# Optimization experiments

Hardware: AMD Instinct MI355X
Metric: run time of the kernel (lower is better)

The kernel has to match this reference:

```python
import jax, jax.numpy as jnp
import numpy as np

K = 3  # kernel size


def _bilinear_sample(x, px, py):
    """Bilinear sample x:[b,c,h,w] at pixel coords px,py:[b,t,h,w].
    Zeros padding, align_corners=True semantics (coords are raw pixel coords).
    Returns [b,c,t,h,w]."""
    b, c, h, w = x.shape
    x0 = jnp.floor(px)
    y0 = jnp.floor(py)
    wx1 = px - x0
    wx0 = 1.0 - wx1
    wy1 = py - y0
    wy0 = 1.0 - wy1
    xf = x.reshape(b, c, h * w)

    def gather(xi, yi):
        valid = (xi >= 0) & (xi <= w - 1) & (yi >= 0) & (yi <= h - 1)
        xi_c = jnp.clip(xi, 0, w - 1).astype(jnp.int32)
        yi_c = jnp.clip(yi, 0, h - 1).astype(jnp.int32)
        idx = (yi_c * w + xi_c).reshape(b, 1, -1)  # [b,1,t*h*w]
        v = jnp.take_along_axis(xf, idx, axis=2).reshape(b, c, *xi.shape[1:])
        return v * valid[:, None].astype(x.dtype)

    out = (gather(x0, y0) * (wx0 * wy0)[:, None]
           + gather(x0 + 1, y0) * (wx1 * wy0)[:, None]
           + gather(x0, y0 + 1) * (wx0 * wy1)[:, None]
           + gather(x0 + 1, y0 + 1) * (wx1 * wy1)[:, None])
    return out


def setup_inputs() -> dict:
    key = jax.random.key(0)
    k1, k2, k3 = jax.random.split(key, 3)
    b, c, h, w = 4, 64, 128, 128
    out_c = 64
    x = jax.random.normal(k1, (b, c, h, w), dtype=jnp.float32)
    offset = jax.random.normal(k2, (b, 2 * K * K, h, w), dtype=jnp.float32)
    weight = jax.random.normal(k3, (out_c, c, K, K), dtype=jnp.float32) * 0.05
    bias = jnp.zeros((out_c,), dtype=jnp.float32)
    return {"x": x, "offset": offset, "weight": weight, "bias": bias}


def reference(x, offset, weight, bias):
    b, c, h, w = x.shape
    kk = K * K
    # base integer grid (x along width, y along height)
    yy, xx = jnp.meshgrid(jnp.arange(h, dtype=x.dtype), jnp.arange(w, dtype=x.dtype), indexing='ij')
    off = offset.reshape(b, kk, 2, h, w)
    # grid_sample with align_corners=True inverts the module's normalization,
    # so effective sampling coords are simply base + offset in pixel space.
    px = xx[None, None] + off[:, :, 0]  # [b,kk,h,w]
    py = yy[None, None] + off[:, :, 1]
    sampled = _bilinear_sample(x, px, py)  # [b,c,kk,h,w]
    w2 = weight.reshape(weight.shape[0], c, kk)  # [o,c,kk]
    out = jnp.einsum('oct,bcthw->bohw', w2, sampled)
    return out + bias[None, :, None, None]
```

## Files before the change

kernel.cpp:

```cpp
#include <hip/hip_runtime.h>
#include <cstddef>

#define BH 4
#define CH 64
#define OH 64
#define HH 128
#define WW 128
#define KK 9
#define HW (HH * WW)

typedef __attribute__((ext_vector_type(8))) short short8;
typedef __attribute__((ext_vector_type(4))) float f32x4;
typedef __attribute__((ext_vector_type(2))) float f32x2;
typedef __attribute__((ext_vector_type(4))) unsigned int uint4v;
typedef __attribute__((ext_vector_type(4))) unsigned short ushort4v;

__device__ __forceinline__ unsigned short f2bf(float f) {
    unsigned u = __float_as_uint(f);
    u += 0x7fffu + ((u >> 16) & 1u);
    return (unsigned short)(u >> 16);
}
__device__ __forceinline__ f32x2 bf2x2(unsigned d) {
    f32x2 r;
    r.x = __uint_as_float(d << 16);
    r.y = __uint_as_float(d & 0xffff0000u);
    return r;
}
__device__ __forceinline__ unsigned pack_bf2(f32x2 v) {
    unsigned u0 = __float_as_uint(v.x);
    u0 += 0x7fffu + ((u0 >> 16) & 1u);
    unsigned u1 = __float_as_uint(v.y);
    u1 += 0x7fffu + ((u1 >> 16) & 1u);
    return __builtin_amdgcn_perm(u1, u0, 0x07060302);
}
__device__ __forceinline__ uint4v combine4(uint4v c00, uint4v c10, uint4v c01, uint4v c11,
                                           float w00, float w10, float w01, float w11) {
    f32x2 W00 = {w00, w00}, W10 = {w10, w10}, W01 = {w01, w01}, W11 = {w11, w11};
    uint4v r;
#pragma unroll
    for (int j = 0; j < 4; ++j) {
        f32x2 s = W00 * bf2x2(c00[j]) + W10 * bf2x2(c10[j])
                + W01 * bf2x2(c01[j]) + W11 * bf2x2(c11[j]);
        r[j] = pack_bf2(s);
    }
    return r;
}

__global__ __launch_bounds__(256) void dcl_prep(const float* __restrict__ x,
                                                const float* __restrict__ wgt,
                                                unsigned short* __restrict__ xt,
                                                unsigned short* __restrict__ wtb) {
    if (blockIdx.x < 1024) {
        __shared__ float tile[64][65];
        int chunk = blockIdx.x;
        int b = chunk >> 8;
        int hw0 = (chunk & 255) * 64;
        int tid = threadIdx.x;
        int tx = tid & 63;
        int ty = tid >> 6;
        const float* xb = x + (size_t)b * CH * HW;
#pragma unroll
        for (int c = ty; c < 64; c += 4)
            tile[c][tx] = xb[(size_t)c * HW + hw0 + tx];
        __syncthreads();
        unsigned short* xtb = xt + ((size_t)b << 20);
        int c4 = (tid & 15) * 4;
        int p0 = tid >> 4;
#pragma unroll
        for (int it = 0; it < 4; ++it) {
            int pxl = p0 + it * 16;
            ushort4v v = { f2bf(tile[c4 + 0][pxl]), f2bf(tile[c4 + 1][pxl]),
                           f2bf(tile[c4 + 2][pxl]), f2bf(tile[c4 + 3][pxl]) };
            *(ushort4v*)(xtb + (size_t)(hw0 + pxl) * CH + c4) = v;
        }
    } else {
        int idx = (blockIdx.x - 1024) * 256 + threadIdx.x;
        int j  = idx & 7;
        int l  = (idx >> 3) & 63;
        int nt = (idx >> 9) & 3;
        int ks = idx >> 11;
        int k = ks * 32 + ((l >> 4) * 8) + j;
        int n = nt * 16 + (l & 15);
        int c = k & 63;
        int t = k >> 6;
        wtb[idx] = f2bf(wgt[(n * CH + c) * KK + t]);
    }
}

#define SMEM_INTS 4352

__global__ __launch_bounds__(256, 4) void dcl_main(
        const unsigned short* __restrict__ xt,
        const float* __restrict__ offset,
        const unsigned short* __restrict__ wtb,
        const float* __restrict__ bias,
        float* __restrict__ out) {
    __shared__ __align__(16) int smem[SMEM_INTS];
    int tid = threadIdx.x;
    int lane = tid & 63;
    int wave = tid >> 6;

    int b  = blockIdx.x >> 8;
    int t8 = blockIdx.x & 255;
    int x0 = (t8 & 7) << 4;
    int y0 = (t8 >> 3) << 2;
    int m = lane & 15;
    int quad = lane >> 4;
    int qoff = quad * 16;
    int y = y0 + wave;
    int pm = x0 + m;

    const char* xtb = (const char*)xt;
    const float* ob = offset + (((size_t)(b * 18)) << 14) + (y << 7) + pm;
    float pxf = (float)pm;
    float pyf = (float)y;

    float oxv[9], oyv[9];
#pragma unroll
    for (int t = 0; t < 9; ++t) {
        oxv[t] = ob[(size_t)(2 * t) << 14];
        oyv[t] = ob[(size_t)(2 * t + 1) << 14];
    }

    const uint4v* bsrc = (const uint4v*)wtb;

    {
        uint4v* dst = (uint4v*)smem;
        dst[tid]       = bsrc[tid];
        dst[tid + 256] = bsrc[tid + 256];
    }

    f32x4 acc[4];
#pragma unroll
    for (int i = 0; i < 4; ++i) acc[i] = (f32x4)(0.f);

    __syncthreads();

#pragma unroll 1
    for (int t = 0; t < 9; ++t) {
        uint4v r0, r1;
        if (t < 8) {
            r0 = bsrc[(t + 1) * 512 + tid];
            r1 = bsrc[(t + 1) * 512 + 256 + tid];
        }

        float fx = pxf + oxv[t];
        float fy = pyf + oyv[t];
        float x0f = floorf(fx), y0f = floorf(fy);
        float wx1 = fx - x0f, wy1 = fy - y0f;
        float wx0 = 1.0f - wx1, wy0 = 1.0f - wy1;
        int ix0 = (int)x0f, iy0 = (int)y0f;
        int ix1 = ix0 + 1, iy1 = iy0 + 1;
        bool vx0 = (unsigned)ix0 < (unsigned)WW;
        bool vx1 = (unsigned)ix1 < (unsigned)WW;
        bool vy0 = (unsigned)iy0 < (unsigned)HH;
        bool vy1 = (unsigned)iy1 < (unsigned)HH;
        float w00 = (vx0 && vy0) ? wx0 * wy0 : 0.0f;
        float w10 = (vx1 && vy0) ? wx1 * wy0 : 0.0f;
        float w01 = (vx0 && vy1) ? wx0 * wy1 : 0.0f;
        float w11 = (vx1 && vy1) ? wx1 * wy1 : 0.0f;
        int cx0 = min(max(ix0, 0), WW - 1), cx1 = min(max(ix1, 0), WW - 1);
        int cy0 = min(max(iy0, 0), HH - 1), cy1 = min(max(iy1, 0), HH - 1);
        int base = b << 14;
        int o00 = ((base + (cy0 << 7) + cx0) << 7) + qoff;
        int o10 = ((base + (cy0 << 7) + cx1) << 7) + qoff;
        int o01 = ((base + (cy1 << 7) + cx0) << 7) + qoff;
        int o11 = ((base + (cy1 << 7) + cx1) << 7) + qoff;

        uint4v c00a = *(const uint4v*)(xtb + o00);
        uint4v c10a = *(const uint4v*)(xtb + o10);
        uint4v c01a = *(const uint4v*)(xtb + o01);
        uint4v c11a = *(const uint4v*)(xtb + o11);
        uint4v c00b = *(const uint4v*)(xtb + o00 + 64);
        uint4v c10b = *(const uint4v*)(xtb + o10 + 64);
        uint4v c01b = *(const uint4v*)(xtb + o01 + 64);
        uint4v c11b = *(const uint4v*)(xtb + o11 + 64);
        uint4v ra = combine4(c00a, c10a, c01a, c11a, w00, w10, w01, w11);
        uint4v rb = combine4(c00b, c10b, c01b, c11b, w00, w10, w01, w11);
        short8 aa = __builtin_bit_cast(short8, ra);
        short8 ab = __builtin_bit_cast(short8, rb);

        const short8* bl = (const short8*)(smem + (t & 1) * 2048);
#pragma unroll
        for (int nt = 0; nt < 4; ++nt)
            acc[nt] = __builtin_amdgcn_mfma_f32_16x16x32_bf16(
                aa, bl[nt * 64 + lane], acc[nt], 0, 0, 0);
#pragma unroll
        for (int nt = 0; nt < 4; ++nt)
            acc[nt] = __builtin_amdgcn_mfma_f32_16x16x32_bf16(
                ab, bl[(4 + nt) * 64 + lane], acc[nt], 0, 0, 0);

        if (t < 8) {
            uint4v* dst = (uint4v*)(smem + ((t + 1) & 1) * 2048);
            dst[tid]       = r0;
            dst[tid + 256] = r1;
        }
        __syncthreads();
    }

    float* o_w = (float*)smem + wave * 1040;
#pragma unroll
    for (int nt = 0; nt < 4; ++nt)
#pragma unroll
        for (int reg = 0; reg < 4; ++reg)
            o_w[(quad * 4 + reg) * 65 + nt * 16 + m] = acc[nt][reg];
    __syncthreads();

    const float* os = (const float*)smem;
#pragma unroll
    for (int j = tid; j < 64 * 64; j += 256) {
        int o = j >> 6;
        int p = j & 63;
        int row = p >> 4, xx = p & 15;
        float v = os[row * 1040 + xx * 65 + o] + bias[o];
        out[(((size_t)(b * OH + o)) << 14) + ((y0 + row) << 7) + x0 + xx] = v;
    }
}

extern "C" void kernel_launch(void* const* d_in, const int* in_sizes, int n_in,
                              void* d_out, int out_size, void* d_ws, size_t ws_size,
                              hipStream_t stream) {
    const float* x      = (const float*)d_in[0];
    const float* offset = (const float*)d_in[1];
    const float* weight = (const float*)d_in[2];
    const float* bias   = (const float*)d_in[3];
    float* out = (float*)d_out;

    unsigned short* xt  = (unsigned short*)d_ws;
    unsigned short* wtb = (unsigned short*)((char*)d_ws + (size_t)BH * HW * CH * 2);

    dcl_prep<<<1024 + 144, 256, 0, stream>>>(x, weight, xt, wtb);
    dcl_main<<<(BH * HW) / 64, 256, 0, stream>>>(xt, offset, wtb, bias, out);
}
```

Measured before the change: 115.8 us.

## Split kernel taps across two wave groups with smem reduction of partial sums

Doubles the block to 512 threads. Two groups of four waves each handle a disjoint subset of the 9 kernel taps for the same 64 pixels: taps 0-4 and taps 5-8. Their partial accumulators are summed in shared memory during the epilogue. Offsets are now loaded one tap ahead instead of all up front, which cuts register pressure. The aim is more latency hiding for the gather loads through higher wave parallelism. The cost is a larger shared memory footprint, a load imbalance (group 1 idles on the last iteration), and an extra reduction.

Result: slower. 148.1 us (+27.9%).

```diff
diff --git a/kernel.cpp b/kernel.cpp
--- a/kernel.cpp
+++ b/kernel.cpp
@@ -87,9 +87,9 @@
     }
 }
 
-#define SMEM_INTS 4352
-
-__global__ __launch_bounds__(256, 4) void dcl_main(
+#define SMEM_INTS 8320
+
+__global__ __launch_bounds__(512, 8) void dcl_main(
         const unsigned short* __restrict__ xt,
         const float* __restrict__ offset,
         const unsigned short* __restrict__ wtb,
@@ -99,6 +99,8 @@
     int tid = threadIdx.x;
     int lane = tid & 63;
     int wave = tid >> 6;
+    int group = wave >> 2;
+    int r = wave & 3;
 
     int b  = blockIdx.x >> 8;
     int t8 = blockIdx.x & 255;
@@ -107,28 +109,25 @@
     int m = lane & 15;
     int quad = lane >> 4;
     int qoff = quad * 16;
-    int y = y0 + wave;
+    int y = y0 + r;
     int pm = x0 + m;
 
     const char* xtb = (const char*)xt;
     const float* ob = offset + (((size_t)(b * 18)) << 14) + (y << 7) + pm;
     float pxf = (float)pm;
     float pyf = (float)y;
-
-    float oxv[9], oyv[9];
-#pragma unroll
-    for (int t = 0; t < 9; ++t) {
-        oxv[t] = ob[(size_t)(2 * t) << 14];
-        oyv[t] = ob[(size_t)(2 * t + 1) << 14];
-    }
+    int t0 = group ? 5 : 0;
 
     const uint4v* bsrc = (const uint4v*)wtb;
 
     {
-        uint4v* dst = (uint4v*)smem;
-        dst[tid]       = bsrc[tid];
-        dst[tid + 256] = bsrc[tid + 256];
-    }
+        uint4v* d0 = (uint4v*)(smem);
+        uint4v* d1 = (uint4v*)(smem + 2 * 2048);
+        d0[tid] = bsrc[0 * 512 + tid];
+        d1[tid] = bsrc[5 * 512 + tid];
+    }
+    float ox_c = ob[(size_t)(2 * t0) << 14];
+    float oy_c = ob[(size_t)(2 * t0 + 1) << 14];
 
     f32x4 acc[4];
 #pragma unroll
@@ -137,64 +136,74 @@
     __syncthreads();
 
 #pragma unroll 1
-    for (int t = 0; t < 9; ++t) {
+    for (int i = 0; i < 5; ++i) {
         uint4v r0, r1;
-        if (t < 8) {
-            r0 = bsrc[(t + 1) * 512 + tid];
-            r1 = bsrc[(t + 1) * 512 + 256 + tid];
-        }
-
-        float fx = pxf + oxv[t];
-        float fy = pyf + oyv[t];
-        float x0f = floorf(fx), y0f = floorf(fy);
-        float wx1 = fx - x0f, wy1 = fy - y0f;
-        float wx0 = 1.0f - wx1, wy0 = 1.0f - wy1;
-        int ix0 = (int)x0f, iy0 = (int)y0f;
-        int ix1 = ix0 + 1, iy1 = iy0 + 1;
-        bool vx0 = (unsigned)ix0 < (unsigned)WW;
-        bool vx1 = (unsigned)ix1 < (unsigned)WW;
-        bool vy0 = (unsigned)iy0 < (unsigned)HH;
-        bool vy1 = (unsigned)iy1 < (unsigned)HH;
-        float w00 = (vx0 && vy0) ? wx0 * wy0 : 0.0f;
-        float w10 = (vx1 && vy0) ? wx1 * wy0 : 0.0f;
-        float w01 = (vx0 && vy1) ? wx0 * wy1 : 0.0f;
-        float w11 = (vx1 && vy1) ? wx1 * wy1 : 0.0f;
-        int cx0 = min(max(ix0, 0), WW - 1), cx1 = min(max(ix1, 0), WW - 1);
-        int cy0 = min(max(iy0, 0), HH - 1), cy1 = min(max(iy1, 0), HH - 1);
-        int base = b << 14;
-        int o00 = ((base + (cy0 << 7) + cx0) << 7) + qoff;
-        int o10 = ((base + (cy0 << 7) + cx1) << 7) + qoff;
-        int o01 = ((base + (cy1 << 7) + cx0) << 7) + qoff;
-        int o11 = ((base + (cy1 << 7) + cx1) << 7) + qoff;
-
-        uint4v c00a = *(const uint4v*)(xtb + o00);
-        uint4v c10a = *(const uint4v*)(xtb + o10);
-        uint4v c01a = *(const uint4v*)(xtb + o01);
-        uint4v c11a = *(const uint4v*)(xtb + o11);
-        uint4v c00b = *(const uint4v*)(xtb + o00 + 64);
-        uint4v c10b = *(const uint4v*)(xtb + o10 + 64);
-        uint4v c01b = *(const uint4v*)(xtb + o01 + 64);
-        uint4v c11b = *(const uint4v*)(xtb + o11 + 64);
-        uint4v ra = combine4(c00a, c10a, c01a, c11a, w00, w10, w01, w11);
-        uint4v rb = combine4(c00b, c10b, c01b, c11b, w00, w10, w01, w11);
-        short8 aa = __builtin_bit_cast(short8, ra);
-        short8 ab = __builtin_bit_cast(short8, rb);
-
-        const short8* bl = (const short8*)(smem + (t & 1) * 2048);
-#pragma unroll
-        for (int nt = 0; nt < 4; ++nt)
-            acc[nt] = __builtin_amdgcn_mfma_f32_16x16x32_bf16(
-                aa, bl[nt * 64 + lane], acc[nt], 0, 0, 0);
-#pragma unroll
-        for (int nt = 0; nt < 4; ++nt)
-            acc[nt] = __builtin_amdgcn_mfma_f32_16x16x32_bf16(
-                ab, bl[(4 + nt) * 64 + lane], acc[nt], 0, 0, 0);
-
-        if (t < 8) {
-            uint4v* dst = (uint4v*)(smem + ((t + 1) & 1) * 2048);
-            dst[tid]       = r0;
-            dst[tid + 256] = r1;
-        }
+        float ox_n = 0.f, oy_n = 0.f;
+        if (i < 4) {
+            r0 = bsrc[(i + 1) * 512 + tid];
+            int tg1 = (6 + i < 9) ? (6 + i) : 8;
+            r1 = bsrc[tg1 * 512 + tid];
+            int tn = t0 + i + 1;
+            if (tn > 8) tn = 8;
+            ox_n = ob[(size_t)(2 * tn) << 14];
+            oy_n = ob[(size_t)(2 * tn + 1) << 14];
+        }
+
+        if (group == 0 || i < 4) {
+            float fx = pxf + ox_c;
+            float fy = pyf + oy_c;
+            float x0f = floorf(fx), y0f = floorf(fy);
+            float wx1 = fx - x0f, wy1 = fy - y0f;
+            float wx0 = 1.0f - wx1, wy0 = 1.0f - wy1;
+            int ix0 = (int)x0f, iy0 = (int)y0f;
+            int ix1 = ix0 + 1, iy1 = iy0 + 1;
+            bool vx0 = (unsigned)ix0 < (unsigned)WW;
+            bool vx1 = (unsigned)ix1 < (unsigned)WW;
+            bool vy0 = (unsigned)iy0 < (unsigned)HH;
+            bool vy1 = (unsigned)iy1 < (unsigned)HH;
+            float w00 = (vx0 && vy0) ? wx0 * wy0 : 0.0f;
+            float w10 = (vx1 && vy0) ? wx1 * wy0 : 0.0f;
+            float w01 = (vx0 && vy1) ? wx0 * wy1 : 0.0f;
+            float w11 = (vx1 && vy1) ? wx1 * wy1 : 0.0f;
+            int cx0 = min(max(ix0, 0), WW - 1), cx1 = min(max(ix1, 0), WW - 1);
+            int cy0 = min(max(iy0, 0), HH - 1), cy1 = min(max(iy1, 0), HH - 1);
+            int base = b << 14;
+            int o00 = ((base + (cy0 << 7) + cx0) << 7) + qoff;
+            int o10 = ((base + (cy0 << 7) + cx1) << 7) + qoff;
+            int o01 = ((base + (cy1 << 7) + cx0) << 7) + qoff;
+            int o11 = ((base + (cy1 << 7) + cx1) << 7) + qoff;
+
+            uint4v c00a = *(const uint4v*)(xtb + o00);
+            uint4v c10a = *(const uint4v*)(xtb + o10);
+            uint4v c01a = *(const uint4v*)(xtb + o01);
+            uint4v c11a = *(const uint4v*)(xtb + o11);
+            uint4v c00b = *(const uint4v*)(xtb + o00 + 64);
+            uint4v c10b = *(const uint4v*)(xtb + o10 + 64);
+            uint4v c01b = *(const uint4v*)(xtb + o01 + 64);
+            uint4v c11b = *(const uint4v*)(xtb + o11 + 64);
+            uint4v ra = combine4(c00a, c10a, c01a, c11a, w00, w10, w01, w11);
+            uint4v rb = combine4(c00b, c10b, c01b, c11b, w00, w10, w01, w11);
+            short8 aa = __builtin_bit_cast(short8, ra);
+            short8 ab = __builtin_bit_cast(short8, rb);
+
+            const short8* bl = (const short8*)(smem + (group * 2 + (i & 1)) * 2048);
+#pragma unroll
+            for (int nt = 0; nt < 4; ++nt)
+                acc[nt] = __builtin_amdgcn_mfma_f32_16x16x32_bf16(
+                    aa, bl[nt * 64 + lane], acc[nt], 0, 0, 0);
+#pragma unroll
+            for (int nt = 0; nt < 4; ++nt)
+                acc[nt] = __builtin_amdgcn_mfma_f32_16x16x32_bf16(
+                    ab, bl[(4 + nt) * 64 + lane], acc[nt], 0, 0, 0);
+        }
+
+        if (i < 4) {
+            int p1 = (i + 1) & 1;
+            ((uint4v*)(smem + (0 + p1) * 2048))[tid] = r0;
+            ((uint4v*)(smem + (2 + p1) * 2048))[tid] = r1;
+        }
+        ox_c = ox_n;
+        oy_c = oy_n;
         __syncthreads();
     }
 
@@ -208,11 +217,12 @@
 
     const float* os = (const float*)smem;
 #pragma unroll
-    for (int j = tid; j < 64 * 64; j += 256) {
+    for (int j = tid; j < 64 * 64; j += 512) {
         int o = j >> 6;
         int p = j & 63;
         int row = p >> 4, xx = p & 15;
-        float v = os[row * 1040 + xx * 65 + o] + bias[o];
+        float v = os[row * 1040 + xx * 65 + o]
+                + os[(row + 4) * 1040 + xx * 65 + o] + bias[o];
         out[(((size_t)(b * OH + o)) << 14) + ((y0 + row) << 7) + x0 + xx] = v;
     }
 }
@@ -230,5 +240,5 @@
     unsigned short* wtb = (unsigned short*)((char*)d_ws + (size_t)BH * HW * CH * 2);
 
     dcl_prep<<<1024 + 144, 256, 0, stream>>>(x, weight, xt, wtb);
-    dcl_main<<<(BH * HW) / 64, 256, 0, stream>>>(xt, offset, wtb, bias, out);
-}
+    dcl_main<<<(BH * HW) / 64, 512, 0, stream>>>(xt, offset, wtb, bias, out);
+}
```

## Stage input halo tile in LDS and read weight fragments directly from global

Applied to the files above, without the earlier changes.

Each block now preloads a 25x13-pixel halo tile of the bf16 channel-last input into shared memory, using a rotated swizzle to avoid bank conflicts. Bilinear corner fetches come from LDS, and a global fallback handles samples whose offsets land outside the tile. Weight fragments, previously double-buffered through LDS with a barrier every tap, are now read straight from global/L2 and the tap loop is fully unrolled with no per-iteration syncs. This trades repeated scattered global gathers for a larger upfront tile load. It risks divergence when offsets exceed the halo, and it raises LDS use to about 41KB per block, which may cut occupancy.

Result: faster. 102.5 us (-11.5%).

```diff
diff --git a/kernel.cpp b/kernel.cpp
--- a/kernel.cpp
+++ b/kernel.cpp
@@ -8,6 +8,13 @@
 #define WW 128
 #define KK 9
 #define HW (HH * WW)
+
+#define HX 4
+#define HY 4
+#define TW 25
+#define TH 13
+#define NREC (TW * TH)
+#define NCHUNK (NREC * 8)
 
 typedef __attribute__((ext_vector_type(8))) short short8;
 typedef __attribute__((ext_vector_type(4))) float f32x4;
@@ -87,15 +94,13 @@
     }
 }
 
-#define SMEM_INTS 4352
-
 __global__ __launch_bounds__(256, 4) void dcl_main(
         const unsigned short* __restrict__ xt,
         const float* __restrict__ offset,
         const unsigned short* __restrict__ wtb,
         const float* __restrict__ bias,
         float* __restrict__ out) {
-    __shared__ __align__(16) int smem[SMEM_INTS];
+    __shared__ __align__(16) int smem[NREC * 32];
     int tid = threadIdx.x;
     int lane = tid & 63;
     int wave = tid >> 6;
@@ -111,6 +116,7 @@
     int pm = x0 + m;
 
     const char* xtb = (const char*)xt;
+    const char* xim = xtb + (((size_t)b << 14) << 7);
     const float* ob = offset + (((size_t)(b * 18)) << 14) + (y << 7) + pm;
     float pxf = (float)pm;
     float pyf = (float)y;
@@ -122,28 +128,30 @@
         oyv[t] = ob[(size_t)(2 * t + 1) << 14];
     }
 
-    const uint4v* bsrc = (const uint4v*)wtb;
-
-    {
-        uint4v* dst = (uint4v*)smem;
-        dst[tid]       = bsrc[tid];
-        dst[tid + 256] = bsrc[tid + 256];
+    uint4v* sv = (uint4v*)smem;
+#pragma unroll
+    for (int i = 0; i < 11; ++i) {
+        int id = tid + i * 256;
+        if (id < NCHUNK) {
+            int p = id >> 3, sub = id & 7;
+            int r = p / TW, col = p - r * TW;
+            int sy = min(max(y0 - HY + r, 0), HH - 1);
+            int sx = min(max(x0 - HX + col, 0), WW - 1);
+            uint4v v = *(const uint4v*)(xim + (((sy << 7) + sx) << 7) + (sub << 4));
+            sv[p * 8 + ((sub + (p & 7)) & 7)] = v;
+        }
     }
 
     f32x4 acc[4];
 #pragma unroll
     for (int i = 0; i < 4; ++i) acc[i] = (f32x4)(0.f);
 
+    const short8* bfrags = (const short8*)wtb;
+
     __syncthreads();
 
-#pragma unroll 1
+#pragma unroll
     for (int t = 0; t < 9; ++t) {
-        uint4v r0, r1;
-        if (t < 8) {
-            r0 = bsrc[(t + 1) * 512 + tid];
-            r1 = bsrc[(t + 1) * 512 + 256 + tid];
-        }
-
         float fx = pxf + oxv[t];
         float fy = pyf + oyv[t];
         float x0f = floorf(fx), y0f = floorf(fy);
@@ -161,43 +169,58 @@
         float w11 = (vx1 && vy1) ? wx1 * wy1 : 0.0f;
         int cx0 = min(max(ix0, 0), WW - 1), cx1 = min(max(ix1, 0), WW - 1);
         int cy0 = min(max(iy0, 0), HH - 1), cy1 = min(max(iy1, 0), HH - 1);
-        int base = b << 14;
-        int o00 = ((base + (cy0 << 7) + cx0) << 7) + qoff;
-        int o10 = ((base + (cy0 << 7) + cx1) << 7) + qoff;
-        int o01 = ((base + (cy1 << 7) + cx0) << 7) + qoff;
-        int o11 = ((base + (cy1 << 7) + cx1) << 7) + qoff;
-
-        uint4v c00a = *(const uint4v*)(xtb + o00);
-        uint4v c10a = *(const uint4v*)(xtb + o10);
-        uint4v c01a = *(const uint4v*)(xtb + o01);
-        uint4v c11a = *(const uint4v*)(xtb + o11);
-        uint4v c00b = *(const uint4v*)(xtb + o00 + 64);
-        uint4v c10b = *(const uint4v*)(xtb + o10 + 64);
-        uint4v c01b = *(const uint4v*)(xtb + o01 + 64);
-        uint4v c11b = *(const uint4v*)(xtb + o11 + 64);
+
+        int lc0 = cx0 - x0 + HX, lc1 = cx1 - x0 + HX;
+        int lr0 = cy0 - y0 + HY, lr1 = cy1 - y0 + HY;
+        bool oof = ((unsigned)lc0 > (TW - 1)) | ((unsigned)lc1 > (TW - 1)) |
+                   ((unsigned)lr0 > (TH - 1)) | ((unsigned)lr1 > (TH - 1));
+        int sc0 = min(max(lc0, 0), TW - 1), sc1 = min(max(lc1, 0), TW - 1);
+        int sr0 = min(max(lr0, 0), TH - 1), sr1 = min(max(lr1, 0), TH - 1);
+        int p00 = sr0 * TW + sc0, p10 = sr0 * TW + sc1;
+        int p01 = sr1 * TW + sc0, p11 = sr1 * TW + sc1;
+
+        uint4v c00a = sv[p00 * 8 + ((quad + (p00 & 7)) & 7)];
+        uint4v c00b = sv[p00 * 8 + ((quad + 4 + (p00 & 7)) & 7)];
+        uint4v c10a = sv[p10 * 8 + ((quad + (p10 & 7)) & 7)];
+        uint4v c10b = sv[p10 * 8 + ((quad + 4 + (p10 & 7)) & 7)];
+        uint4v c01a = sv[p01 * 8 + ((quad + (p01 & 7)) & 7)];
+        uint4v c01b = sv[p01 * 8 + ((quad + 4 + (p01 & 7)) & 7)];
+        uint4v c11a = sv[p11 * 8 + ((quad + (p11 & 7)) & 7)];
+        uint4v c11b = sv[p11 * 8 + ((quad + 4 + (p11 & 7)) & 7)];
+
+        if (__builtin_expect(oof, 0)) {
+            int base = b << 14;
+            int o00 = ((base + (cy0 << 7) + cx0) << 7) + qoff;
+            int o10 = ((base + (cy0 << 7) + cx1) << 7) + qoff;
+            int o01 = ((base + (cy1 << 7) + cx0) << 7) + qoff;
+            int o11 = ((base + (cy1 << 7) + cx1) << 7) + qoff;
+            c00a = *(const uint4v*)(xtb + o00);
+            c00b = *(const uint4v*)(xtb + o00 + 64);
+            c10a = *(const uint4v*)(xtb + o10);
+            c10b = *(const uint4v*)(xtb + o10 + 64);
+            c01a = *(const uint4v*)(xtb + o01);
+            c01b = *(const uint4v*)(xtb + o01 + 64);
+            c11a = *(const uint4v*)(xtb + o11);
+            c11b = *(const uint4v*)(xtb + o11 + 64);
+        }
+
         uint4v ra = combine4(c00a, c10a, c01a, c11a, w00, w10, w01, w11);
         uint4v rb = combine4(c00b, c10b, c01b, c11b, w00, w10, w01, w11);
         short8 aa = __builtin_bit_cast(short8, ra);
         short8 ab = __builtin_bit_cast(short8, rb);
 
-        const short8* bl = (const short8*)(smem + (t & 1) * 2048);
+        int ks = 2 * t;
 #pragma unroll
         for (int nt = 0; nt < 4; ++nt)
             acc[nt] = __builtin_amdgcn_mfma_f32_16x16x32_bf16(
-                aa, bl[nt * 64 + lane], acc[nt], 0, 0, 0);
+                aa, bfrags[(ks * 4 + nt) * 64 + lane], acc[nt], 0, 0, 0);
 #pragma unroll
         for (int nt = 0; nt < 4; ++nt)
             acc[nt] = __builtin_amdgcn_mfma_f32_16x16x32_bf16(
-                ab, bl[(4 + nt) * 64 + lane], acc[nt], 0, 0, 0);
-
-        if (t < 8) {
-            uint4v* dst = (uint4v*)(smem + ((t + 1) & 1) * 2048);
-            dst[tid]       = r0;
-            dst[tid + 256] = r1;
-        }
-        __syncthreads();
-    }
-
+                ab, bfrags[((ks + 1) * 4 + nt) * 64 + lane], acc[nt], 0, 0, 0);
+    }
+
+    __syncthreads();
     float* o_w = (float*)smem + wave * 1040;
 #pragma unroll
     for (int nt = 0; nt < 4; ++nt)
```
